# Kernel tuning notes

Hardware: AMD Instinct MI355X
Metric: run time of the kernel (lower is better)

The kernel has to match this reference:

```python
import jax, jax.numpy as jnp
import numpy as np

D = 512       # feature dim of X0 (Linear(512,...) in emb)
DQK = D // 8  # SAGAN-style reduced query/key dim
B = 256
S = 255       # structured features -> N = S + 1 tokens


def _lin(key, fan_in, fan_out):
    kw, kb = jax.random.split(key)
    s = 1.0 / np.sqrt(fan_in)
    W = jax.random.uniform(kw, (fan_in, fan_out), jnp.float32, -s, s)
    b = jax.random.uniform(kb, (fan_out,), jnp.float32, -s, s)
    return W, b


def setup_inputs() -> dict:
    key = jax.random.key(0)
    ks = jax.random.split(key, 9)
    X0 = jax.random.normal(ks[0], (B, D), jnp.float32)
    X_struc = jax.random.normal(ks[1], (B, S), jnp.float32)
    Wq, bq = _lin(ks[2], D, DQK)
    Wk, bk = _lin(ks[3], D, DQK)
    Wv, bv = _lin(ks[4], D, D)
    gamma = jnp.zeros((), jnp.float32) + 0.5  # nonzero so attention path contributes
    W1, b1 = _lin(ks[5], D, 1024)
    W2, b2 = _lin(ks[6], 1024, 512)
    W3, b3 = _lin(ks[7], 512, 128)
    return {"X0": X0, "X_struc": X_struc, "Wq": Wq, "bq": bq, "Wk": Wk, "bk": bk,
            "Wv": Wv, "bv": bv, "gamma": gamma, "W1": W1, "b1": b1,
            "W2": W2, "b2": b2, "W3": W3, "b3": b3}


def reference(X0, X_struc, Wq, bq, Wk, bk, Wv, bv, gamma, W1, b1, W2, b2, W3, b3):
    # Batched outer product replaces the per-sample torch.mm loop:
    # X1[b, s, d] = X_struc[b, s] * X0[b, d]
    X1 = X_struc[:, :, None] * X0[:, None, :]            # [B, S, D]
    X = jnp.concatenate([X0[:, None, :], X1], axis=1)    # [B, N, D], N = S+1
    # SAGAN-style self-attention (Self_Attention(out_planes=512))
    Q = X @ Wq + bq                                      # [B, N, DQK]
    K = X @ Wk + bk                                      # [B, N, DQK]
    V = X @ Wv + bv                                      # [B, N, D]
    A = jax.nn.softmax(jnp.einsum('bnc,bmc->bnm', Q, K), axis=-1)  # [B, N, N]
    Y = gamma * jnp.einsum('bnm,bmd->bnd', A, V) + X     # residual
    # emb MLP: 512 -> 1024 -> 512 -> 128, ReLU after each layer
    h = jax.nn.relu(Y @ W1 + b1)
    h = jax.nn.relu(h @ W2 + b2)
    out = jax.nn.relu(h @ W3 + b3)                       # [B, N, 128]
    return out
```

## Files before the change

### kernel.cpp

```cpp
#include <hip/hip_runtime.h>
#include <hip/hip_bf16.h>

typedef __attribute__((ext_vector_type(8))) short s16x8;
typedef __attribute__((ext_vector_type(16))) float f32x16;

__device__ __forceinline__ unsigned short f2bfu(float x) {
  __hip_bfloat16 b = __float2bfloat16(x);
  return *reinterpret_cast<unsigned short*>(&b);
}

__device__ __forceinline__ unsigned int cvtpk(float a, float b) {
  unsigned int r;
  asm("v_cvt_pk_bf16_f32 %0, %1, %2" : "=v"(r) : "v"(a), "v"(b));
  return r;
}

__global__ __launch_bounds__(256) void prep1_k(
    const float* __restrict__ W2, const float* __restrict__ W3,
    const float* __restrict__ W1,
    unsigned short* __restrict__ W2P, unsigned short* __restrict__ W3P,
    unsigned short* __restrict__ W1P,
    const float* __restrict__ X0, const float* __restrict__ Wv,
    const float* __restrict__ Wq, const float* __restrict__ Wk,
    float* __restrict__ V0ws, float* __restrict__ QKws) {
  __shared__ __align__(16) char smc[65664];
  const int tid = threadIdx.x;
  const int blk = blockIdx.x;

  if (blk < 64) {
    unsigned short* lt = (unsigned short*)smc;
    if (blk < 32) {
      const int kb = blk;
#pragma unroll
      for (int i = 0; i < 16; ++i) {
        const int e4 = i * 256 + tid;
        const int r = e4 >> 7, c4 = (e4 & 127) * 4;
        const float4 v = *(const float4*)(W2 + (size_t)(kb * 32 + r) * 512 + c4);
        lt[r * 514 + c4 + 0] = f2bfu(v.x);
        lt[r * 514 + c4 + 1] = f2bfu(v.y);
        lt[r * 514 + c4 + 2] = f2bfu(v.z);
        lt[r * 514 + c4 + 3] = f2bfu(v.w);
      }
      __syncthreads();
#pragma unroll
      for (int i = 0; i < 8; ++i) {
        const int c = i * 256 + tid;
        const int kgl = c >> 10, nb = (c >> 6) & 15, l = c & 63;
        const int col = nb * 32 + (l & 31);
        const int k0 = kgl * 16 + (l >> 5) * 8;
        s16x8 v;
#pragma unroll
        for (int j = 0; j < 8; ++j) v[j] = lt[(k0 + j) * 514 + col];
        *(s16x8*)(W2P + ((size_t)((kb * 2 + kgl) * 16 + nb) * 64 + l) * 8) = v;
      }
    } else if (blk < 48) {
      const int kb = blk - 32;
#pragma unroll
      for (int i = 0; i < 32; ++i) {
        const int e4 = i * 256 + tid;
        const int r = e4 >> 8, c4 = (e4 & 255) * 4;
        const float4 v = *(const float4*)(W1 + (size_t)(kb * 32 + r) * 1024 + c4);
        lt[r * 1026 + c4 + 0] = f2bfu(v.x);
        lt[r * 1026 + c4 + 1] = f2bfu(v.y);
        lt[r * 1026 + c4 + 2] = f2bfu(v.z);
        lt[r * 1026 + c4 + 3] = f2bfu(v.w);
      }
      __syncthreads();
#pragma unroll
      for (int i = 0; i < 16; ++i) {
        const int c = i * 256 + tid;
        const int kgl = c >> 11, nb = (c >> 6) & 31, l = c & 63;
        const int col = nb * 32 + (l & 31);
        const int k0 = kgl * 16 + (l >> 5) * 8;
        s16x8 v;
#pragma unroll
        for (int j = 0; j < 8; ++j) v[j] = lt[(k0 + j) * 1026 + col];
        *(s16x8*)(W1P + ((size_t)((kb * 2 + kgl) * 32 + nb) * 64 + l) * 8) = v;
      }
    } else {
      const int kb = blk - 48;
#pragma unroll
      for (int i = 0; i < 4; ++i) {
        const int e4 = i * 256 + tid;
        const int r = e4 >> 5, c4 = (e4 & 31) * 4;
        const float4 v = *(const float4*)(W3 + (size_t)(kb * 32 + r) * 128 + c4);
        lt[r * 130 + c4 + 0] = f2bfu(v.x);
        lt[r * 130 + c4 + 1] = f2bfu(v.y);
        lt[r * 130 + c4 + 2] = f2bfu(v.z);
        lt[r * 130 + c4 + 3] = f2bfu(v.w);
      }
      __syncthreads();
#pragma unroll
      for (int i = 0; i < 2; ++i) {
        const int c = i * 256 + tid;
        const int kgl = c >> 8, nb = (c >> 6) & 3, l = c & 63;
        const int col = nb * 32 + (l & 31);
        const int k0 = kgl * 16 + (l >> 5) * 8;
        s16x8 v;
#pragma unroll
        for (int j = 0; j < 8; ++j) v[j] = lt[(k0 + j) * 130 + col];
        *(s16x8*)(W3P + ((size_t)((kb * 2 + kgl) * 4 + nb) * 64 + l) * 8) = v;
      }
    }
    return;
  }
  float* As = (float*)smc;
  float* Bs = (float*)(smc + 2176);
  const int r = blk - 64;
  const int bn = r % 10, bm = r / 10;
  const int tx = tid & 15, ty = tid >> 4;
  float acc[2][4] = {};
  for (int k0 = 0; k0 < 512; k0 += 16) {
    if (tid < 128) {
      const int row = tid >> 2, kk = (tid & 3) * 4;
      const float4 v = *(const float4*)(X0 + (size_t)(bm * 32 + row) * 512 + k0 + kk);
      As[row * 17 + kk] = v.x; As[row * 17 + kk + 1] = v.y;
      As[row * 17 + kk + 2] = v.z; As[row * 17 + kk + 3] = v.w;
    }
    {
      const int k = tid >> 4, n4 = (tid & 15) * 4;
      float4 v;
      if (bn < 8)       v = *(const float4*)(Wv + (size_t)(k0 + k) * 512 + bn * 64 + n4);
      else if (bn == 8) v = *(const float4*)(Wq + (size_t)(k0 + k) * 64 + n4);
      else              v = *(const float4*)(Wk + (size_t)(k0 + k) * 64 + n4);
      Bs[k * 68 + n4] = v.x; Bs[k * 68 + n4 + 1] = v.y;
      Bs[k * 68 + n4 + 2] = v.z; Bs[k * 68 + n4 + 3] = v.w;
    }
    __syncthreads();
#pragma unroll
    for (int kk = 0; kk < 16; ++kk) {
      float a[2], bb[4];
#pragma unroll
      for (int i = 0; i < 2; ++i) a[i] = As[(ty * 2 + i) * 17 + kk];
#pragma unroll
      for (int j = 0; j < 4; ++j) bb[j] = Bs[kk * 68 + tx * 4 + j];
#pragma unroll
      for (int i = 0; i < 2; ++i)
#pragma unroll
        for (int j = 0; j < 4; ++j) acc[i][j] = fmaf(a[i], bb[j], acc[i][j]);
    }
    __syncthreads();
  }
#pragma unroll
  for (int i = 0; i < 2; ++i) {
    const int row = bm * 32 + ty * 2 + i;
#pragma unroll
    for (int j = 0; j < 4; ++j) {
      const int n = tx * 4 + j;
      if (bn < 8)       V0ws[(size_t)row * 512 + bn * 64 + n] = acc[i][j];
      else if (bn == 8) QKws[(size_t)row * 128 + n] = acc[i][j];
      else              QKws[(size_t)row * 128 + 64 + n] = acc[i][j];
    }
  }
}

__global__ __launch_bounds__(256) void prep2_k(
    const float* __restrict__ Xs, const float* __restrict__ QKws,
    const float* __restrict__ bq, float* __restrict__ Wws,
    const float* __restrict__ V0ws, const float* __restrict__ X0,
    const float* __restrict__ bv, const float* __restrict__ W1,
    const unsigned short* __restrict__ W1P,
    const float* __restrict__ gp, const float* __restrict__ b1,
    float* __restrict__ Pws, float* __restrict__ Rws, float* __restrict__ Cws) {
  const int tid = threadIdx.x;
  if (blockIdx.x < 256) {
    const int b = blockIdx.x, t = tid;
    __shared__ float sv[256];
    __shared__ float scal[4];
    sv[t] = (t == 0) ? 1.0f : Xs[b * 255 + t - 1];
    __syncthreads();
    if (t == 0) {
      float al = 0, g2 = 0;
      for (int j = 0; j < 64; ++j) {
        al = fmaf(QKws[b * 128 + j], QKws[b * 128 + 64 + j], al);
        g2 = fmaf(bq[j], QKws[b * 128 + 64 + j], g2);
      }
      float mx = sv[0], mn = sv[0];
      for (int m2 = 1; m2 < 256; ++m2) { mx = fmaxf(mx, sv[m2]); mn = fminf(mn, sv[m2]); }
      scal[0] = al; scal[1] = g2; scal[2] = mx; scal[3] = mn;
    }
    __syncthreads();
    const float c = fmaf(scal[0], sv[tid], scal[1]);
    const float M = (c >= 0.f) ? c * scal[2] : c * scal[3];
    float Z = 0, Wm = 0;
    for (int m2 = 0; m2 < 256; ++m2) {
      const float e = __expf(fmaf(c, sv[m2], -M));
      Z += e;
      Wm = fmaf(sv[m2], e, Wm);
    }
    Wws[b * 256 + tid] = Wm / Z;
    return;
  }
  if (blockIdx.x < 260) {
    const int col = (blockIdx.x - 256) * 256 + tid;
    float a = 0;
    for (int d = 0; d < 512; ++d) a = fmaf(bv[d], W1[(size_t)d * 1024 + col], a);
    Cws[col] = fmaf(gp[0], a, b1[col]);
    return;
  }
  const int r = blockIdx.x - 260;
  const int pr = r >> 6;
  const int rem = r & 63;
  const int mb = rem >> 4, nb = rem & 15;
  const float* srcA = pr ? X0 : V0ws;
  float* dst = pr ? Rws : Pws;
  const int lane = tid & 63, w = tid >> 6;
  const int la31 = lane & 31, hi = lane >> 5;
  const int rowbase = mb * 64 + (w >> 1) * 32;
  const int nbW = nb * 2 + (w & 1);
  const float* ar = srcA + (size_t)(rowbase + la31) * 512 + hi * 8;
  const unsigned short* pBW = W1P + ((size_t)nbW * 64 + lane) * 8;

  f32x16 acc;
#pragma unroll
  for (int i = 0; i < 16; ++i) acc[i] = 0.f;

  float4 fa[2][2];
  s16x8 bst[2];
  fa[0][0] = *(const float4*)(ar);
  fa[0][1] = *(const float4*)(ar + 4);
  bst[0] = *(const s16x8*)(pBW);
  pBW += 16384;

#pragma unroll 2
  for (int kg = 0; kg < 32; ++kg) {
    const int par = kg & 1;
    if (kg < 31) {
      fa[par ^ 1][0] = *(const float4*)(ar + (kg + 1) * 16);
      fa[par ^ 1][1] = *(const float4*)(ar + (kg + 1) * 16 + 4);
      bst[par ^ 1] = *(const s16x8*)(pBW);
      pBW += 16384;
    }
    union { s16x8 v; unsigned int u[4]; } t;
    const float4 a0 = fa[par][0], a1 = fa[par][1];
    t.u[0] = cvtpk(a0.x, a0.y);
    t.u[1] = cvtpk(a0.z, a0.w);
    t.u[2] = cvtpk(a1.x, a1.y);
    t.u[3] = cvtpk(a1.z, a1.w);
    acc = __builtin_amdgcn_mfma_f32_32x32x16_bf16(t.v, bst[par], acc, 0, 0, 0);
  }
#pragma unroll
  for (int reg = 0; reg < 16; ++reg) {
    const int rowl = (reg & 3) + 8 * (reg >> 2) + 4 * hi;
    dst[(size_t)(rowbase + rowl) * 1024 + nbW * 32 + la31] = acc[reg];
  }
}

__global__ __launch_bounds__(512, 2) void fused_k(
    const float* __restrict__ Xs, const float* __restrict__ gp,
    const unsigned short* __restrict__ W2P,
    const float* __restrict__ b2,
    const unsigned short* __restrict__ W3P,
    const float* __restrict__ b3,
    const float* __restrict__ Cws, const float* __restrict__ Wws,
    const float* __restrict__ Pws, const float* __restrict__ Rws,
    float* __restrict__ out)
{
  __shared__ __align__(16) unsigned char sm[143360];
  unsigned short* smU = (unsigned short*)sm;
  float* PRC = (float*)(sm + 131072);
  const int tid = threadIdx.x;
  const int lane = tid & 63, wid = tid >> 6;
  const int la31 = lane & 31, hi = lane >> 5;
  const int m0 = blockIdx.x * 128;
  const int b = m0 >> 8;
  const float g = gp[0];

  const int rg = tid & 127, kslot = tid >> 7;
  const int tokg = (m0 & 255) + rg;
  const float gw = g * Wws[b * 256 + tokg];
  const float sr = (tokg == 0) ? 1.0f : Xs[b * 255 + tokg - 1];

#pragma unroll
  for (int i = 0; i < 6; ++i) {
    const int idx = i * 512 + tid;
    float v;
    if (idx < 1024)      v = Pws[b * 1024 + idx];
    else if (idx < 2048) v = Rws[b * 1024 + (idx - 1024)];
    else                 v = Cws[idx - 2048];
    PRC[idx] = v;
  }

  auto gen = [&](int buf, int step) {
    const int kb = step * 64 + kslot * 16;
    float e[16];
#pragma unroll
    for (int j = 0; j < 16; j += 4) {
      const float4 Pv = *(const float4*)(PRC + kb + j);
      const float4 Rv = *(const float4*)(PRC + 1024 + kb + j);
      const float4 Cv = *(const float4*)(PRC + 2048 + kb + j);
      e[j + 0] = fmaxf(fmaf(gw, Pv.x, fmaf(sr, Rv.x, Cv.x)), 0.f);
      e[j + 1] = fmaxf(fmaf(gw, Pv.y, fmaf(sr, Rv.y, Cv.y)), 0.f);
      e[j + 2] = fmaxf(fmaf(gw, Pv.z, fmaf(sr, Rv.z, Cv.z)), 0.f);
      e[j + 3] = fmaxf(fmaf(gw, Pv.w, fmaf(sr, Rv.w, Cv.w)), 0.f);
    }
    union { s16x8 v; unsigned int u[4]; } t0, t1;
    t0.u[0] = cvtpk(e[0], e[1]);  t0.u[1] = cvtpk(e[2], e[3]);
    t0.u[2] = cvtpk(e[4], e[5]);  t0.u[3] = cvtpk(e[6], e[7]);
    t1.u[0] = cvtpk(e[8], e[9]);  t1.u[1] = cvtpk(e[10], e[11]);
    t1.u[2] = cvtpk(e[12], e[13]); t1.u[3] = cvtpk(e[14], e[15]);
    *(s16x8*)(sm + buf * 16384 + ((kslot * 2 + 0) * 128 + rg) * 16) = t0.v;
    *(s16x8*)(sm + buf * 16384 + ((kslot * 2 + 1) * 128 + rg) * 16) = t1.v;
  };

  f32x16 acc[4][2];
#pragma unroll
  for (int mf = 0; mf < 4; ++mf)
#pragma unroll
    for (int nf = 0; nf < 2; ++nf)
#pragma unroll
      for (int i = 0; i < 16; ++i) acc[mf][nf][i] = 0.f;

  const unsigned short* pB = W2P + ((size_t)(wid * 2) * 64 + lane) * 8;
  s16x8 bst[2][2];
#pragma unroll
  for (int nf = 0; nf < 2; ++nf)
    bst[0][nf] = *(const s16x8*)(pB + nf * 512);
  pB += 8192;

  __syncthreads();
  gen(0, 0);

  for (int step = 0; step < 16; ++step) {
    __syncthreads();
    if (step < 15) gen((step + 1) & 1, step + 1);
    const int abase = (step & 1) * 16384;
#pragma unroll
    for (int kgl = 0; kgl < 4; ++kgl) {
      const int par = kgl & 1;
#pragma unroll
      for (int nf = 0; nf < 2; ++nf)
        bst[par ^ 1][nf] = *(const s16x8*)(pB + nf * 512);
      pB += 8192;
      s16x8 af[4];
#pragma unroll
      for (int mf = 0; mf < 4; ++mf)
        af[mf] = *(const s16x8*)(sm + abase + ((kgl * 2 + hi) * 128 + mf * 32 + la31) * 16);
#pragma unroll
      for (int nf = 0; nf < 2; ++nf)
#pragma unroll
        for (int mf = 0; mf < 4; ++mf)
          acc[mf][nf] = __builtin_amdgcn_mfma_f32_32x32x16_bf16(af[mf], bst[par][nf], acc[mf][nf], 0, 0, 0);
    }
  }
  __syncthreads();

#pragma unroll
  for (int nf = 0; nf < 2; ++nf) {
    const int col = wid * 64 + nf * 32 + la31;
    const float bb = b2[col];
    const int sc = col >> 3, c7 = col & 7;
#pragma unroll
    for (int mf = 0; mf < 4; ++mf) {
#pragma unroll
      for (int reg = 0; reg < 16; ++reg) {
        const int row = mf * 32 + (reg & 3) + 8 * (reg >> 2) + 4 * hi;
        const int sp = (sc & 56) | ((sc ^ row) & 7);
        smU[row * 512 + sp * 8 + c7] = f2bfu(fmaxf(acc[mf][nf][reg] + bb, 0.f));
      }
    }
  }
  __syncthreads();

  const int wr = wid >> 2, wc = wid & 3;
  f32x16 acc2[2];
#pragma unroll
  for (int m = 0; m < 2; ++m)
#pragma unroll
    for (int i = 0; i < 16; ++i) acc2[m][i] = 0.f;

  const unsigned short* pW = W3P + ((size_t)wc * 64 + lane) * 8;
  s16x8 wst[2];
  wst[0] = *(const s16x8*)(pW);
  pW += 2048;
#pragma unroll 2
  for (int kg = 0; kg < 32; ++kg) {
    const int par = kg & 1;
    wst[par ^ 1] = *(const s16x8*)(pW);
    pW += 2048;
    const int s = kg * 2 + hi;
#pragma unroll
    for (int m = 0; m < 2; ++m) {
      const int row = wr * 64 + m * 32 + la31;
      const int sp = (s & 56) | ((s ^ row) & 7);
      const s16x8 afh = *(const s16x8*)(&sm[row * 1024 + (sp << 4)]);
      acc2[m] = __builtin_amdgcn_mfma_f32_32x32x16_bf16(afh, wst[par], acc2[m], 0, 0, 0);
    }
  }

  {
    const int cB = wc * 32 + la31;
    const float b3v = b3[cB];
#pragma unroll
    for (int m = 0; m < 2; ++m)
#pragma unroll
      for (int reg = 0; reg < 16; ++reg) {
        const int row = m0 + wr * 64 + m * 32 + (reg & 3) + 8 * (reg >> 2) + 4 * hi;
        out[(size_t)row * 128 + cB] = fmaxf(acc2[m][reg] + b3v, 0.f);
      }
  }
}

extern "C" void kernel_launch(void* const* d_in, const int* in_sizes, int n_in,
                              void* d_out, int out_size, void* d_ws, size_t ws_size,
                              hipStream_t stream) {
  const float* X0 = (const float*)d_in[0];
  const float* Xs = (const float*)d_in[1];
  const float* Wq = (const float*)d_in[2];
  const float* bq = (const float*)d_in[3];
  const float* Wk = (const float*)d_in[4];
  const float* bk = (const float*)d_in[5];
  const float* Wv = (const float*)d_in[6];
  const float* bv = (const float*)d_in[7];
  const float* gp = (const float*)d_in[8];
  const float* W1 = (const float*)d_in[9];
  const float* b1 = (const float*)d_in[10];
  const float* W2 = (const float*)d_in[11];
  const float* b2 = (const float*)d_in[12];
  const float* W3 = (const float*)d_in[13];
  const float* b3 = (const float*)d_in[14];

  char* ws = (char*)d_ws;
  float* Cws = (float*)(ws);
  float* Wws = (float*)(ws + 4096);
  float* Pws = (float*)(ws + 266240);
  float* Rws = (float*)(ws + 1314816);
  unsigned short* W2P = (unsigned short*)(ws + 2363392);
  unsigned short* W3P = (unsigned short*)(ws + 3411968);
  float* V0ws = (float*)(ws + 3543040);
  float* QKws = (float*)(ws + 4067328);
  unsigned short* W1P = (unsigned short*)(ws + 4198400);
  float* out = (float*)d_out;

  hipLaunchKernelGGL(prep1_k, dim3(144), dim3(256), 0, stream,
                     W2, W3, W1, W2P, W3P, W1P, X0, Wv, Wq, Wk, V0ws, QKws);
  hipLaunchKernelGGL(prep2_k, dim3(388), dim3(256), 0, stream,
                     Xs, QKws, bq, Wws, V0ws, X0, bv, W1, W1P, gp, b1, Pws, Rws, Cws);
  hipLaunchKernelGGL(fused_k, dim3(512), dim3(512), 0, stream,
                     Xs, gp, W2P, b2, W3P, b3, Cws, Wws, Pws, Rws, out);
}
```

Measured before the change: 138.7 us.

## Halve fused kernel row tile to 64 rows for higher occupancy

The fused MLP kernel now processes 64 token rows per block instead of 128 and launches twice as many blocks. Shared memory drops from 140KB to 64KB and accumulator registers are halved, and the launch bound asks for 4 blocks per CU. The A-generation and both GEMM stages are rewritten for the smaller tile. The aim is more resident waves and better latency hiding, but each block now reads the full W2/W3 weights for half as many rows, which doubles weight traffic per output row.

```diff
diff --git a/kernel.cpp b/kernel.cpp
--- a/kernel.cpp
+++ b/kernel.cpp
@@ -246,7 +246,7 @@
   }
 }
 
-__global__ __launch_bounds__(512, 2) void fused_k(
+__global__ __launch_bounds__(512, 4) void fused_k(
     const float* __restrict__ Xs, const float* __restrict__ gp,
     const unsigned short* __restrict__ W2P,
     const float* __restrict__ b2,
@@ -256,17 +256,17 @@
     const float* __restrict__ Pws, const float* __restrict__ Rws,
     float* __restrict__ out)
 {
-  __shared__ __align__(16) unsigned char sm[143360];
+  __shared__ __align__(16) unsigned char sm[65536];
   unsigned short* smU = (unsigned short*)sm;
-  float* PRC = (float*)(sm + 131072);
+  float* PRC = (float*)(sm + 16384);
   const int tid = threadIdx.x;
   const int lane = tid & 63, wid = tid >> 6;
   const int la31 = lane & 31, hi = lane >> 5;
-  const int m0 = blockIdx.x * 128;
-  const int b = m0 >> 8;
+  const int m0 = blockIdx.x * 64;
+  const int b = blockIdx.x >> 2;
   const float g = gp[0];
 
-  const int rg = tid & 127, kslot = tid >> 7;
+  const int rg = lane;
   const int tokg = (m0 & 255) + rg;
   const float gw = g * Wws[b * 256 + tokg];
   const float sr = (tokg == 0) ? 1.0f : Xs[b * 255 + tokg - 1];
@@ -282,10 +282,10 @@
   }
 
   auto gen = [&](int buf, int step) {
-    const int kb = step * 64 + kslot * 16;
-    float e[16];
-#pragma unroll
-    for (int j = 0; j < 16; j += 4) {
+    const int kb = step * 64 + wid * 8;
+    float e[8];
+#pragma unroll
+    for (int j = 0; j < 8; j += 4) {
       const float4 Pv = *(const float4*)(PRC + kb + j);
       const float4 Rv = *(const float4*)(PRC + 1024 + kb + j);
       const float4 Cv = *(const float4*)(PRC + 2048 + kb + j);
@@ -294,18 +294,15 @@
       e[j + 2] = fmaxf(fmaf(gw, Pv.z, fmaf(sr, Rv.z, Cv.z)), 0.f);
       e[j + 3] = fmaxf(fmaf(gw, Pv.w, fmaf(sr, Rv.w, Cv.w)), 0.f);
     }
-    union { s16x8 v; unsigned int u[4]; } t0, t1;
+    union { s16x8 v; unsigned int u[4]; } t0;
     t0.u[0] = cvtpk(e[0], e[1]);  t0.u[1] = cvtpk(e[2], e[3]);
     t0.u[2] = cvtpk(e[4], e[5]);  t0.u[3] = cvtpk(e[6], e[7]);
-    t1.u[0] = cvtpk(e[8], e[9]);  t1.u[1] = cvtpk(e[10], e[11]);
-    t1.u[2] = cvtpk(e[12], e[13]); t1.u[3] = cvtpk(e[14], e[15]);
-    *(s16x8*)(sm + buf * 16384 + ((kslot * 2 + 0) * 128 + rg) * 16) = t0.v;
-    *(s16x8*)(sm + buf * 16384 + ((kslot * 2 + 1) * 128 + rg) * 16) = t1.v;
+    *(s16x8*)(sm + buf * 8192 + (wid * 64 + rg) * 16) = t0.v;
   };
 
-  f32x16 acc[4][2];
-#pragma unroll
-  for (int mf = 0; mf < 4; ++mf)
+  f32x16 acc[2][2];
+#pragma unroll
+  for (int mf = 0; mf < 2; ++mf)
 #pragma unroll
     for (int nf = 0; nf < 2; ++nf)
 #pragma unroll
@@ -324,7 +321,7 @@
   for (int step = 0; step < 16; ++step) {
     __syncthreads();
     if (step < 15) gen((step + 1) & 1, step + 1);
-    const int abase = (step & 1) * 16384;
+    const int abase = (step & 1) * 8192;
 #pragma unroll
     for (int kgl = 0; kgl < 4; ++kgl) {
       const int par = kgl & 1;
@@ -332,14 +329,14 @@
       for (int nf = 0; nf < 2; ++nf)
         bst[par ^ 1][nf] = *(const s16x8*)(pB + nf * 512);
       pB += 8192;
-      s16x8 af[4];
-#pragma unroll
-      for (int mf = 0; mf < 4; ++mf)
-        af[mf] = *(const s16x8*)(sm + abase + ((kgl * 2 + hi) * 128 + mf * 32 + la31) * 16);
+      s16x8 af[2];
+#pragma unroll
+      for (int mf = 0; mf < 2; ++mf)
+        af[mf] = *(const s16x8*)(sm + abase + ((kgl * 2 + hi) * 64 + mf * 32 + la31) * 16);
 #pragma unroll
       for (int nf = 0; nf < 2; ++nf)
 #pragma unroll
-        for (int mf = 0; mf < 4; ++mf)
+        for (int mf = 0; mf < 2; ++mf)
           acc[mf][nf] = __builtin_amdgcn_mfma_f32_32x32x16_bf16(af[mf], bst[par][nf], acc[mf][nf], 0, 0, 0);
     }
   }
@@ -351,7 +348,7 @@
     const float bb = b2[col];
     const int sc = col >> 3, c7 = col & 7;
 #pragma unroll
-    for (int mf = 0; mf < 4; ++mf) {
+    for (int mf = 0; mf < 2; ++mf) {
 #pragma unroll
       for (int reg = 0; reg < 16; ++reg) {
         const int row = mf * 32 + (reg & 3) + 8 * (reg >> 2) + 4 * hi;
@@ -363,11 +360,9 @@
   __syncthreads();
 
   const int wr = wid >> 2, wc = wid & 3;
-  f32x16 acc2[2];
-#pragma unroll
-  for (int m = 0; m < 2; ++m)
-#pragma unroll
-    for (int i = 0; i < 16; ++i) acc2[m][i] = 0.f;
+  f32x16 acc2;
+#pragma unroll
+  for (int i = 0; i < 16; ++i) acc2[i] = 0.f;
 
   const unsigned short* pW = W3P + ((size_t)wc * 64 + lane) * 8;
   s16x8 wst[2];
@@ -379,25 +374,20 @@
     wst[par ^ 1] = *(const s16x8*)(pW);
     pW += 2048;
     const int s = kg * 2 + hi;
-#pragma unroll
-    for (int m = 0; m < 2; ++m) {
-      const int row = wr * 64 + m * 32 + la31;
-      const int sp = (s & 56) | ((s ^ row) & 7);
-      const s16x8 afh = *(const s16x8*)(&sm[row * 1024 + (sp << 4)]);
-      acc2[m] = __builtin_amdgcn_mfma_f32_32x32x16_bf16(afh, wst[par], acc2[m], 0, 0, 0);
-    }
+    const int row = wr * 32 + la31;
+    const int sp = (s & 56) | ((s ^ row) & 7);
+    const s16x8 afh = *(const s16x8*)(&sm[row * 1024 + (sp << 4)]);
+    acc2 = __builtin_amdgcn_mfma_f32_32x32x16_bf16(afh, wst[par], acc2, 0, 0, 0);
   }
 
   {
     const int cB = wc * 32 + la31;
     const float b3v = b3[cB];
 #pragma unroll
-    for (int m = 0; m < 2; ++m)
-#pragma unroll
-      for (int reg = 0; reg < 16; ++reg) {
-        const int row = m0 + wr * 64 + m * 32 + (reg & 3) + 8 * (reg >> 2) + 4 * hi;
-        out[(size_t)row * 128 + cB] = fmaxf(acc2[m][reg] + b3v, 0.f);
-      }
+    for (int reg = 0; reg < 16; ++reg) {
+      const int row = m0 + wr * 32 + (reg & 3) + 8 * (reg >> 2) + 4 * hi;
+      out[(size_t)row * 128 + cB] = fmaxf(acc2[reg] + b3v, 0.f);
+    }
   }
 }
 
@@ -436,6 +426,6 @@
                      W2, W3, W1, W2P, W3P, W1P, X0, Wv, Wq, Wk, V0ws, QKws);
   hipLaunchKernelGGL(prep2_k, dim3(388), dim3(256), 0, stream,
                      Xs, QKws, bq, Wws, V0ws, X0, bv, W1, W1P, gp, b1, Pws, Rws, Cws);
-  hipLaunchKernelGGL(fused_k, dim3(512), dim3(512), 0, stream,
+  hipLaunchKernelGGL(fused_k, dim3(1024), dim3(512), 0, stream,
                      Xs, gp, W2P, b2, W3P, b3, Cws, Wws, Pws, Rws, out);
 }
```

Result: faster. 133.3 us (-3.9%).
